# Optimization experiments

Measured on AMD Instinct MI355X. Metric: run time of the kernel, lower is better.

The kernel has to match this reference:

```python
import jax, jax.numpy as jnp
import numpy as np

N = 50000      # nodes
E = 800000     # edges (avg degree 16)
F_IN = 128
HID = 64
NCLS = 40
K = 2          # num_stacks
T = 2          # num_layers (shared weights)


def setup_inputs() -> dict:
    key = jax.random.key(0)
    ks = jax.random.split(key, 10)
    s = 0.05
    return {
        "x": jax.random.normal(ks[0], (N, F_IN), dtype=jnp.float32),
        "edge_index": jax.random.randint(ks[1], (2, E), 0, N),
        "w1_init": jax.random.normal(ks[2], (K, F_IN, HID), dtype=jnp.float32) * s,
        "w1": jax.random.normal(ks[3], (K, HID, HID), dtype=jnp.float32) * s,
        "v1": jax.random.normal(ks[4], (K, F_IN, HID), dtype=jnp.float32) * s,
        "b1": jax.random.normal(ks[5], (K, HID), dtype=jnp.float32) * s,
        "w2_init": jax.random.normal(ks[6], (K, HID, NCLS), dtype=jnp.float32) * s,
        "w2": jax.random.normal(ks[7], (K, NCLS, NCLS), dtype=jnp.float32) * s,
        "v2": jax.random.normal(ks[8], (K, HID, NCLS), dtype=jnp.float32) * s,
        "b2": jax.random.normal(ks[9], (K, NCLS), dtype=jnp.float32) * s,
    }


def _gcn_norm(src, dst, n):
    # PyG gcn_norm with add_self_loops=False: deg over destination, sym norm
    deg = jax.ops.segment_sum(jnp.ones_like(dst, dtype=jnp.float32), dst, num_segments=n)
    dinv = jnp.where(deg > 0, 1.0 / jnp.sqrt(deg), 0.0)
    return dinv[src] * dinv[dst]  # [E]


def _arma_conv(x, src, dst, norm, n, w_init, w, v, b, act):
    # x: [N, Fin]; w_init: [K, Fin, Fout]; w: [K, Fout, Fout]; v: [K, Fin, Fout]; b: [K, Fout]
    root = jnp.einsum('nf,kfg->kng', x, v)  # [K, N, Fout], dropout=0 -> identity
    out = None
    for t in range(T):
        if t == 0:
            h = jnp.einsum('nf,kfg->kng', x, w_init)
        else:
            h = jnp.einsum('knf,kfg->kng', out, w)
        # sparse neighbor aggregation: out[i] = sum_{(j->i)} norm_e * h[j]
        agg = jax.vmap(
            lambda hk: jax.ops.segment_sum(hk[src] * norm[:, None], dst, num_segments=n)
        )(h)  # [K, N, Fout]
        out = act(agg + root + b[:, None, :])
    return out.mean(axis=0)  # mean over stacks -> [N, Fout]


def reference(x, edge_index, w1_init, w1, v1, b1, w2_init, w2, v2, b2):
    src, dst = edge_index[0], edge_index[1]
    norm = _gcn_norm(src, dst, N)
    h = _arma_conv(x, src, dst, norm, N, w1_init, w1, v1, b1, jax.nn.relu)
    h = jax.nn.relu(h)  # wrapper ReLU; dropout is identity in eval
    o = _arma_conv(h, src, dst, norm, N, w2_init, w2, v2, b2, lambda z: z)
    return jax.nn.log_softmax(o, axis=1)
```

## Files before the change

kernel.cpp:

```cpp
#include <hip/hip_runtime.h>
#include <hip/hip_bf16.h>
#include <math.h>

#define N_NODES 50000
#define F_IN 128
#define HID 64
#define NCLS 40
#define K_STACKS 2
#define SCAN_TILE 1024
#define NBLK_CNT 256

typedef __attribute__((ext_vector_type(8))) short short8;
typedef __attribute__((ext_vector_type(4))) float floatx4;
typedef __attribute__((ext_vector_type(2))) float floatx2;

__device__ __forceinline__ unsigned int f32_to_bf16_bits(float f) {
    unsigned int u = __float_as_uint(f);
    return (u + 0x7fffu + ((u >> 16) & 1u)) >> 16;
}
__device__ __forceinline__ unsigned int pack_bf16x2(float a, float b) {
    return f32_to_bf16_bits(a) | (f32_to_bf16_bits(b) << 16);
}
__device__ __forceinline__ unsigned char f32_to_fp8(float v) {
    int pk = __builtin_amdgcn_cvt_pk_fp8_f32(v, v, 0, false);
    return (unsigned char)(pk & 0xff);
}


__global__ __launch_bounds__(256) void count_kernel(const int* __restrict__ dst,
                                                    int* __restrict__ counts,
                                                    int* __restrict__ tileSums, int E) {
    __shared__ int hist[256];
    __shared__ int ts[64];
    int blk = blockIdx.x, t = threadIdx.x;
    hist[t] = 0;
    if (t < 64) ts[t] = 0;
    __syncthreads();
    int chunk = (E + NBLK_CNT - 1) / NBLK_CNT;
    int s = blk * chunk, e = min(E, s + chunk);
    for (int i = s + t; i < e; i += 256) atomicAdd(&hist[dst[i] >> 8], 1);
    __syncthreads();
    counts[t * NBLK_CNT + blk] = hist[t];
    atomicAdd(&ts[t >> 2], hist[t]);
    __syncthreads();
    if (t < 64) atomicAdd(&tileSums[t], ts[t]);
}

__global__ __launch_bounds__(256) void scan_phase3_excl(const int* __restrict__ in,
                                                        const int* __restrict__ tileSums,
                                                        int* __restrict__ out, int n) {
    __shared__ int lds[256];
    __shared__ int tsum[64];
    int b = blockIdx.x, t = threadIdx.x;
    if (t < 64) tsum[t] = tileSums[t];
    int base = b * SCAN_TILE + t * 4;
    int e[4];
    int s = 0;
#pragma unroll
    for (int i = 0; i < 4; ++i) {
        e[i] = (base + i < n) ? in[base + i] : 0;
        s += e[i];
    }
    lds[t] = s;
    __syncthreads();
    int v = s;
    for (int off = 1; off < 256; off <<= 1) {
        int add = (t >= off) ? lds[t - off] : 0;
        __syncthreads();
        v += add;
        lds[t] = v;
        __syncthreads();
    }
    int toff = 0;
    for (int i = 0; i < b; ++i) toff += tsum[i];
    int run = (t == 0 ? 0 : lds[t - 1]) + toff;
#pragma unroll
    for (int i = 0; i < 4; ++i) {
        if (base + i < n) {
            out[base + i] = run;
            run += e[i];
        }
    }
}

__global__ __launch_bounds__(256) void bucket_scatter_kernel(const int* __restrict__ src,
                                                             const int* __restrict__ dst,
                                                             const int* __restrict__ scanned,
                                                             unsigned int* __restrict__ pairs,
                                                             int E) {
    __shared__ int cur[256];
    int blk = blockIdx.x, t = threadIdx.x;
    cur[t] = scanned[t * NBLK_CNT + blk];
    __syncthreads();
    int chunk = (E + NBLK_CNT - 1) / NBLK_CNT;
    int s0 = blk * chunk, e0 = min(E, s0 + chunk);
    for (int i = s0 + t; i < e0; i += 256) {
        int d = dst[i];
        int pos = atomicAdd(&cur[d >> 8], 1);
        pairs[pos] = (unsigned int)src[i] | ((unsigned int)(d & 255) << 16);
    }
}

__global__ __launch_bounds__(256) void csr_build_kernel(const unsigned int* __restrict__ pairs,
                                                        const int* __restrict__ scanned,
                                                        int* __restrict__ row_ptr,
                                                        float* __restrict__ dinv,
                                                        int* __restrict__ col, int N, int E) {
    __shared__ int degl[256], lds[256], curl[256], sb[2];
    int b = blockIdx.x, t = threadIdx.x;
    if (t == 0) {
        sb[0] = scanned[b * NBLK_CNT];
        sb[1] = (b + 1 < 256) ? scanned[(b + 1) * NBLK_CNT] : E;
    }
    degl[t] = 0;
    __syncthreads();
    int bstart = sb[0], bend = sb[1];
    for (int e = bstart + t; e < bend; e += 256) {
        atomicAdd(&degl[(pairs[e] >> 16) & 255], 1);
    }
    __syncthreads();
    int d = degl[t];
    lds[t] = d;
    __syncthreads();
    int v = d;
    for (int off = 1; off < 256; off <<= 1) {
        int add = (t >= off) ? lds[t - off] : 0;
        __syncthreads();
        v += add;
        lds[t] = v;
        __syncthreads();
    }
    int excl = v - d;
    int node = b * 256 + t;
    if (node <= N) row_ptr[node] = bstart + excl;
    if (node < N) dinv[node] = (d > 0) ? (1.0f / sqrtf((float)d)) : 0.0f;
    curl[t] = excl;
    __syncthreads();
    for (int e = bstart + t; e < bend; e += 256) {
        unsigned int p = pairs[e];
        int ln = (p >> 16) & 255;
        int pos = atomicAdd(&curl[ln], 1);
        col[bstart + pos] = (int)(p & 0xffffu);
    }
}

__device__ __forceinline__ void wt_one(const float* __restrict__ in,
                                       unsigned short* __restrict__ out, int li, int C, int F,
                                       int CP) {
    int k = li / (F * CP);
    int r = li - k * F * CP;
    int f = r / CP;
    int c = r - f * CP;
    out[li] = (c < C) ? (unsigned short)f32_to_bf16_bits(in[((size_t)k * C + c) * F + f]) : 0;
}

__global__ void wt_all_kernel(const float* v1, const float* w1i, const float* w1,
                              const float* v2, const float* w2i, const float* w2,
                              unsigned short* v1t, unsigned short* w1it, unsigned short* w1t,
                              unsigned short* v2t, unsigned short* w2it, unsigned short* w2t) {
    int i = blockIdx.x * blockDim.x + threadIdx.x;
    if (i < 16384) wt_one(v1, v1t, i, 128, 64, 128);
    else if (i < 32768) wt_one(w1i, w1it, i - 16384, 128, 64, 128);
    else if (i < 40960) wt_one(w1, w1t, i - 32768, 64, 64, 64);
    else if (i < 46080) wt_one(v2, v2t, i - 40960, 64, 40, 64);
    else if (i < 51200) wt_one(w2i, w2it, i - 46080, 64, 40, 64);
    else if (i < 56320) wt_one(w2, w2t, i - 51200, 40, 40, 64);
}

template <int CINP>
__device__ __forceinline__ void stage_A(const void* A, unsigned short* At, size_t abase,
                                        int n0, int t, int N, int CREAL, int a_bf16) {
    constexpr int CP8 = CINP / 8;
    constexpr int MS = CP8 - 1;
    constexpr int SH = (CP8 == 16) ? 4 : 3;
    for (int i = t; i < 64 * CP8; i += 256) {
        int n = i >> SH;
        int c = i & MS;
        uint4 w = make_uint4(0u, 0u, 0u, 0u);
        int gn = n0 + n;
        if (gn < N && c * 8 < CREAL) {
            if (a_bf16) {
                w = *(const uint4*)((const unsigned short*)A + abase + (size_t)gn * CREAL + c * 8);
            } else {
                const float* srcp = (const float*)A + abase + (size_t)gn * CREAL + c * 8;
                float4 f0 = *(const float4*)(srcp);
                float4 f1 = *(const float4*)(srcp + 4);
                w.x = pack_bf16x2(f0.x, f0.y);
                w.y = pack_bf16x2(f0.z, f0.w);
                w.z = pack_bf16x2(f1.x, f1.y);
                w.w = pack_bf16x2(f1.z, f1.w);
            }
        }
        *(uint4*)(At + n * CINP + ((c ^ (n & MS)) << 3)) = w;
    }
}

template <int CINP>
__device__ __forceinline__ void stage_B(const unsigned short* Bk, unsigned short* Bs, int t,
                                        int COUT) {
    constexpr int CP8 = CINP / 8;
    constexpr int MS = CP8 - 1;
    constexpr int SH = (CP8 == 16) ? 4 : 3;
    for (int i = t; i < COUT * CP8; i += 256) {
        int f = i >> SH;
        int c = i & MS;
        uint4 w = *(const uint4*)(Bk + f * CINP + c * 8);
        *(uint4*)(Bs + f * CINP + ((c ^ (f & MS)) << 3)) = w;
    }
}

template <int CINP>
__global__ __launch_bounds__(256) void gemm_mfma(
    const void* __restrict__ A, const unsigned short* __restrict__ Bt,
    void* __restrict__ out, const float* __restrict__ scale, int N, int COUT, int CREAL,
    int a_per_k, int a_bf16, int out_fp8, int do_scale, int out_inter) {
    constexpr int MS = CINP / 8 - 1;
    __shared__ __align__(16) unsigned short At[64 * CINP];
    __shared__ __align__(16) unsigned short Bs[64 * CINP];

    const int k = blockIdx.y;
    const int n0 = blockIdx.x * 64;
    const int t = threadIdx.x;
    stage_A<CINP>(A, At, a_per_k ? (size_t)k * N * CREAL : (size_t)0, n0, t, N, CREAL, a_bf16);
    stage_B<CINP>(Bt + (size_t)k * COUT * CINP, Bs, t, COUT);
    __syncthreads();

    const int lane = t & 63;
    const int wv = t >> 6;
    const int quad = lane >> 4;
    const int li = lane & 15;
    const int m0 = wv * 16;

    floatx4 acc[4] = {{0.f, 0.f, 0.f, 0.f}, {0.f, 0.f, 0.f, 0.f},
                      {0.f, 0.f, 0.f, 0.f}, {0.f, 0.f, 0.f, 0.f}};
    const int am = (m0 + li) & MS;
#pragma unroll
    for (int kc = 0; kc < CINP / 32; ++kc) {
        int cc = kc * 4 + quad;
        short8 a = *(const short8*)(At + (m0 + li) * CINP + ((cc ^ am) << 3));
#pragma unroll
        for (int nt = 0; nt < 4; ++nt) {
            if (nt * 16 < COUT) {
                int f = nt * 16 + li;
                short8 b = *(const short8*)(Bs + f * CINP + ((cc ^ (f & MS)) << 3));
                acc[nt] = __builtin_amdgcn_mfma_f32_16x16x32_bf16(a, b, acc[nt], 0, 0, 0);
            }
        }
    }

    float sc[4] = {1.f, 1.f, 1.f, 1.f};
    if (do_scale) {
#pragma unroll
        for (int r = 0; r < 4; ++r) {
            int node = n0 + m0 + quad * 4 + r;
            sc[r] = (node < N) ? scale[node] : 1.f;
        }
    }
#pragma unroll
    for (int nt = 0; nt < 4; ++nt) {
        if (nt * 16 >= COUT) continue;
        int f = nt * 16 + li;
        if (f >= COUT) continue;
#pragma unroll
        for (int r = 0; r < 4; ++r) {
            int node = n0 + m0 + quad * 4 + r;
            if (node < N) {
                float val = acc[nt][r] * sc[r];
                if (out_inter) {
                    size_t o = (size_t)node * 2 * COUT + (size_t)k * COUT + f;
                    if (out_fp8)
                        ((unsigned char*)out)[o] = f32_to_fp8(val);
                    else
                        ((unsigned short*)out)[o] = (unsigned short)f32_to_bf16_bits(val);
                } else {
                    size_t o = ((size_t)k * N + node) * COUT + f;
                    ((float*)out)[o] = val;
                }
            }
        }
    }
}

template <int CINP>
__global__ __launch_bounds__(256) void gemm2_mfma(
    const void* __restrict__ A, const unsigned short* __restrict__ Bt1,
    const unsigned short* __restrict__ Bt2, unsigned short* __restrict__ out1,
    unsigned char* __restrict__ out2, const float* __restrict__ scale, int N, int COUT,
    int CREAL, int a_bf16) {
    constexpr int MS = CINP / 8 - 1;
    __shared__ __align__(16) unsigned short At[64 * CINP];
    __shared__ __align__(16) unsigned short Bs1[64 * CINP];
    __shared__ __align__(16) unsigned short Bs2[64 * CINP];

    const int k = blockIdx.y;
    const int n0 = blockIdx.x * 64;
    const int t = threadIdx.x;
    stage_A<CINP>(A, At, (size_t)0, n0, t, N, CREAL, a_bf16);
    stage_B<CINP>(Bt1 + (size_t)k * COUT * CINP, Bs1, t, COUT);
    stage_B<CINP>(Bt2 + (size_t)k * COUT * CINP, Bs2, t, COUT);
    __syncthreads();

    const int lane = t & 63;
    const int wv = t >> 6;
    const int quad = lane >> 4;
    const int li = lane & 15;
    const int m0 = wv * 16;

    floatx4 acc1[4] = {{0.f, 0.f, 0.f, 0.f}, {0.f, 0.f, 0.f, 0.f},
                       {0.f, 0.f, 0.f, 0.f}, {0.f, 0.f, 0.f, 0.f}};
    floatx4 acc2[4] = {{0.f, 0.f, 0.f, 0.f}, {0.f, 0.f, 0.f, 0.f},
                       {0.f, 0.f, 0.f, 0.f}, {0.f, 0.f, 0.f, 0.f}};
    const int am = (m0 + li) & MS;
#pragma unroll
    for (int kc = 0; kc < CINP / 32; ++kc) {
        int cc = kc * 4 + quad;
        short8 a = *(const short8*)(At + (m0 + li) * CINP + ((cc ^ am) << 3));
#pragma unroll
        for (int nt = 0; nt < 4; ++nt) {
            if (nt * 16 < COUT) {
                int f = nt * 16 + li;
                int bo = f * CINP + ((cc ^ (f & MS)) << 3);
                short8 b1 = *(const short8*)(Bs1 + bo);
                short8 b2 = *(const short8*)(Bs2 + bo);
                acc1[nt] = __builtin_amdgcn_mfma_f32_16x16x32_bf16(a, b1, acc1[nt], 0, 0, 0);
                acc2[nt] = __builtin_amdgcn_mfma_f32_16x16x32_bf16(a, b2, acc2[nt], 0, 0, 0);
            }
        }
    }

    float sc[4];
#pragma unroll
    for (int r = 0; r < 4; ++r) {
        int node = n0 + m0 + quad * 4 + r;
        sc[r] = (node < N) ? scale[node] : 1.f;
    }
#pragma unroll
    for (int nt = 0; nt < 4; ++nt) {
        if (nt * 16 >= COUT) continue;
        int f = nt * 16 + li;
        if (f >= COUT) continue;
#pragma unroll
        for (int r = 0; r < 4; ++r) {
            int node = n0 + m0 + quad * 4 + r;
            if (node < N) {
                out1[((size_t)k * N + node) * COUT + f] =
                    (unsigned short)f32_to_bf16_bits(acc1[nt][r]);
                out2[(size_t)node * 2 * COUT + (size_t)k * COUT + f] =
                    f32_to_fp8(acc2[nt][r] * sc[r]);
            }
        }
    }
}

template <int F>
__global__ __launch_bounds__(256) void agg_kernel(
    const unsigned char* __restrict__ h8, const int* __restrict__ row_ptr,
    const int* __restrict__ col, const float* __restrict__ dinv,
    const unsigned short* __restrict__ rootb, const float* __restrict__ bias,
    void* __restrict__ out, int N, int do_relu, int mode) {
    constexpr int FH = F / 8;
    constexpr int ROWB = 2 * F;
    int wid = (blockIdx.x * blockDim.x + threadIdx.x) >> 6;
    int lane = threadIdx.x & 63;
    int half = lane >> 5;
    int l32 = lane & 31;
    int node = wid * 2 + half;
    bool valid = node < N;
    int e0 = 0, deg = 0;
    float dv = 0.f;
    if (valid) {
        e0 = row_ptr[node];
        deg = row_ptr[node + 1] - e0;
        dv = dinv[node];
    }
    const int sub = l32 >> 4;
    const int fq = l32 & 15;
    const int kk = fq >> 3;
    const int fqq = fq & 7;
    const int fqc = (fqq < FH) ? fqq : (FH - 1);
    const int foff = kk * F + fqc * 8;

    float acc[8] = {};
    for (int w0 = 0; w0 < deg; w0 += 32) {
        int mye = w0 + l32;
        int c = (mye < deg) ? col[e0 + mye] : 0;
        int nch = min(deg - w0, 32);
        for (int base = 0; base < nch; base += 16) {
            uint2 v[8];
            float wj[8];
#pragma unroll
            for (int u = 0; u < 8; ++u) {
                int j = base + u * 2 + sub;
                int cj = __shfl(c, (half << 5) | (j & 31));
                bool ok = (j < nch);
                wj[u] = ok ? 1.f : 0.f;
                int cs = ok ? cj : 0;
                v[u] = *(const uint2*)(h8 + (size_t)cs * ROWB + foff);
            }
#pragma unroll
            for (int u = 0; u < 8; ++u) {
                floatx2 f0 = __builtin_amdgcn_cvt_pk_f32_fp8(v[u].x, false);
                floatx2 f1 = __builtin_amdgcn_cvt_pk_f32_fp8(v[u].x, true);
                floatx2 f2 = __builtin_amdgcn_cvt_pk_f32_fp8(v[u].y, false);
                floatx2 f3 = __builtin_amdgcn_cvt_pk_f32_fp8(v[u].y, true);
                acc[0] += wj[u] * f0.x;
                acc[1] += wj[u] * f0.y;
                acc[2] += wj[u] * f1.x;
                acc[3] += wj[u] * f1.y;
                acc[4] += wj[u] * f2.x;
                acc[5] += wj[u] * f2.y;
                acc[6] += wj[u] * f3.x;
                acc[7] += wj[u] * f3.y;
            }
        }
    }
#pragma unroll
    for (int i = 0; i < 8; ++i) acc[i] += __shfl_xor(acc[i], 16);

    size_t oc = ((size_t)kk * N + (valid ? node : 0)) * F + fqc * 8;
    uint4 rv = *(const uint4*)(rootb + oc);
    const float* bp = bias + kk * F + fqc * 8;
    float4 b0 = *(const float4*)(bp);
    float4 b1 = *(const float4*)(bp + 4);
    const unsigned int ru[4] = {rv.x, rv.y, rv.z, rv.w};
    float res[8];
#pragma unroll
    for (int q = 0; q < 4; ++q) {
        float rlo = __uint_as_float(ru[q] << 16);
        float rhi = __uint_as_float(ru[q] & 0xffff0000u);
        float blo = (q < 2) ? ((q == 0) ? b0.x : b0.z) : ((q == 2) ? b1.x : b1.z);
        float bhi = (q < 2) ? ((q == 0) ? b0.y : b0.w) : ((q == 2) ? b1.y : b1.w);
        res[2 * q] = acc[2 * q] * dv + rlo + blo;
        res[2 * q + 1] = acc[2 * q + 1] * dv + rhi + bhi;
    }
    if (do_relu) {
#pragma unroll
        for (int i = 0; i < 8; ++i) res[i] = fmaxf(res[i], 0.f);
    }
    if (mode == 0) {
        if (sub == 0 && fqq < FH && valid) {
            size_t o = ((size_t)kk * N + node) * F + fqq * 8;
            uint4 w;
            w.x = pack_bf16x2(res[0], res[1]);
            w.y = pack_bf16x2(res[2], res[3]);
            w.z = pack_bf16x2(res[4], res[5]);
            w.w = pack_bf16x2(res[6], res[7]);
            *(uint4*)((unsigned short*)out + o) = w;
        }
    } else {
        float mres[8];
#pragma unroll
        for (int i = 0; i < 8; ++i) mres[i] = 0.5f * (res[i] + __shfl_xor(res[i], 8));
        if (mode == 1) {
            if (sub == 0 && kk == 0 && fqq < FH && valid) {
                size_t o = (size_t)node * F + fqq * 8;
                *(float4*)((float*)out + o) = make_float4(mres[0], mres[1], mres[2], mres[3]);
                *(float4*)((float*)out + o + 4) = make_float4(mres[4], mres[5], mres[6], mres[7]);
            }
        } else {
            bool act = (fqq < FH);
            float lm = -INFINITY;
            if (act) {
#pragma unroll
                for (int i = 0; i < 8; ++i) lm = fmaxf(lm, mres[i]);
            }
#pragma unroll
            for (int m = 1; m < 8; m <<= 1) lm = fmaxf(lm, __shfl_xor(lm, m));
            float ls = 0.f;
            if (act) {
#pragma unroll
                for (int i = 0; i < 8; ++i) ls += expf(mres[i] - lm);
            }
#pragma unroll
            for (int m = 1; m < 8; m <<= 1) ls += __shfl_xor(ls, m);
            float lg = lm + logf(ls);
            if (sub == 0 && kk == 0 && act && valid) {
                size_t o = (size_t)node * F + fqq * 8;
                *(float4*)((float*)out + o) =
                    make_float4(mres[0] - lg, mres[1] - lg, mres[2] - lg, mres[3] - lg);
                *(float4*)((float*)out + o + 4) =
                    make_float4(mres[4] - lg, mres[5] - lg, mres[6] - lg, mres[7] - lg);
            }
        }
    }
}


static inline size_t align256(size_t x) { return (x + 255) & ~(size_t)255; }

extern "C" void kernel_launch(void* const* d_in, const int* in_sizes, int n_in,
                              void* d_out, int out_size, void* d_ws, size_t ws_size,
                              hipStream_t stream) {
    const float* x = (const float*)d_in[0];
    const int* ei = (const int*)d_in[1];
    const float* w1_init = (const float*)d_in[2];
    const float* w1 = (const float*)d_in[3];
    const float* v1 = (const float*)d_in[4];
    const float* b1 = (const float*)d_in[5];
    const float* w2_init = (const float*)d_in[6];
    const float* w2 = (const float*)d_in[7];
    const float* v2 = (const float*)d_in[8];
    const float* b2 = (const float*)d_in[9];

    const int N = in_sizes[0] / F_IN;
    const int E = in_sizes[1] / 2;
    const int* src = ei;
    const int* dst = ei + E;

    char* p = (char*)d_ws;
    auto take = [&](size_t bytes) {
        char* r = p;
        p += align256(bytes);
        return r;
    };
    float* dinv = (float*)take((size_t)N * 4);
    int* row_ptr = (int*)take((size_t)(N + 1) * 4);
    int* tileSums = (int*)take(256 * 4);
    int* counts = (int*)take((size_t)256 * NBLK_CNT * 4);
    int* scanned = (int*)take((size_t)256 * NBLK_CNT * 4);
    unsigned int* pairs = (unsigned int*)take((size_t)E * 4);
    int* col = (int*)take((size_t)E * 4);
    unsigned short* v1t = (unsigned short*)take((size_t)2 * 64 * 128 * 2);
    unsigned short* w1it = (unsigned short*)take((size_t)2 * 64 * 128 * 2);
    unsigned short* w1t = (unsigned short*)take((size_t)2 * 64 * 64 * 2);
    unsigned short* v2t = (unsigned short*)take((size_t)2 * 40 * 64 * 2);
    unsigned short* w2it = (unsigned short*)take((size_t)2 * 40 * 64 * 2);
    unsigned short* w2t = (unsigned short*)take((size_t)2 * 40 * 64 * 2);
    unsigned short* rootb = (unsigned short*)take((size_t)K_STACKS * N * HID * 2);
    unsigned char* hb8 = (unsigned char*)take((size_t)K_STACKS * N * HID);
    unsigned short* hc = (unsigned short*)take((size_t)K_STACKS * N * HID * 2);
    float* h1 = (float*)take((size_t)N * HID * 4);

    const int TB = 256;
    const int nCnt = 256 * NBLK_CNT;
    const int nScanBlocks = nCnt / SCAN_TILE;
    const int nBuckets = (N + 255) / 256;
    const int ntiles = (N + 63) / 64;

    hipMemsetAsync(tileSums, 0, 256, stream);
    count_kernel<<<NBLK_CNT, 256, 0, stream>>>(dst, counts, tileSums, E);
    scan_phase3_excl<<<nScanBlocks, 256, 0, stream>>>(counts, tileSums, scanned, nCnt);
    bucket_scatter_kernel<<<NBLK_CNT, 256, 0, stream>>>(src, dst, scanned, pairs, E);
    csr_build_kernel<<<nBuckets, 256, 0, stream>>>(pairs, scanned, row_ptr, dinv, col, N, E);

    wt_all_kernel<<<(56320 + TB - 1) / TB, TB, 0, stream>>>(v1, w1_init, w1, v2, w2_init, w2,
                                                            v1t, w1it, w1t, v2t, w2it, w2t);

    dim3 ggrid(ntiles, K_STACKS);
    const int agg_blocks = ((N + 1) / 2 + 3) / 4;

    gemm2_mfma<128><<<ggrid, 256, 0, stream>>>(x, v1t, w1it, rootb, hb8, dinv, N, HID, 128, 0);
    agg_kernel<HID><<<agg_blocks, 256, 0, stream>>>(hb8, row_ptr, col, dinv, rootb, b1, hc, N, 1, 0);
    gemm_mfma<64><<<ggrid, 256, 0, stream>>>(hc, w1t, hb8, dinv, N, HID, 64, 1, 1, 1, 1, 1);
    agg_kernel<HID><<<agg_blocks, 256, 0, stream>>>(hb8, row_ptr, col, dinv, rootb, b1, h1, N, 1, 1);

    gemm2_mfma<64><<<ggrid, 256, 0, stream>>>(h1, v2t, w2it, rootb, hb8, dinv, N, NCLS, 64, 0);
    agg_kernel<NCLS><<<agg_blocks, 256, 0, stream>>>(hb8, row_ptr, col, dinv, rootb, b2, hc, N, 0, 0);
    gemm_mfma<64><<<ggrid, 256, 0, stream>>>(hc, w2t, hb8, dinv, N, NCLS, 40, 1, 1, 1, 1, 1);
    agg_kernel<NCLS><<<agg_blocks, 256, 0, stream>>>(hb8, row_ptr, col, dinv, rootb, b2,
                                                     (float*)d_out, N, 0, 2);
}
```

Before: 283.3 us.

## Fuse sparse aggregation with following dense GEMMs into per-tile kernels

Replaces separate aggregation and GEMM launches with agg_gemm kernels that gather neighbors for a 64-node tile, apply bias/ReLU (and stack mean), write the result to shared memory as bf16, and then run the next MFMA GEMM in the same block. The first GEMM now loops over both stacks inside a block instead of using a 2D grid, so the A tile is staged once. This removes the intermediate bf16/fp32 round trips through global memory and cuts the launch count from eight to five. In exchange, the aggregation now uses 64-node blocks with more shared memory, which may lower occupancy and load balance for the irregular gather.

```diff
diff --git a/kernel.cpp b/kernel.cpp
--- a/kernel.cpp
+++ b/kernel.cpp
@@ -209,115 +209,39 @@
     }
 }
 
-template <int CINP>
-__global__ __launch_bounds__(256) void gemm_mfma(
-    const void* __restrict__ A, const unsigned short* __restrict__ Bt,
-    void* __restrict__ out, const float* __restrict__ scale, int N, int COUT, int CREAL,
-    int a_per_k, int a_bf16, int out_fp8, int do_scale, int out_inter) {
-    constexpr int MS = CINP / 8 - 1;
+__global__ __launch_bounds__(256) void gemm12_kernel(
+    const float* __restrict__ A, const unsigned short* __restrict__ Bt1,
+    const unsigned short* __restrict__ Bt2, unsigned short* __restrict__ out1,
+    unsigned char* __restrict__ out2, const float* __restrict__ scale, int N) {
+    constexpr int CINP = 128;
+    constexpr int MS = 15;
     __shared__ __align__(16) unsigned short At[64 * CINP];
-    __shared__ __align__(16) unsigned short Bs[64 * CINP];
-
-    const int k = blockIdx.y;
+    __shared__ __align__(16) unsigned short Bs1[64 * CINP];
+    __shared__ __align__(16) unsigned short Bs2[64 * CINP];
     const int n0 = blockIdx.x * 64;
     const int t = threadIdx.x;
-    stage_A<CINP>(A, At, a_per_k ? (size_t)k * N * CREAL : (size_t)0, n0, t, N, CREAL, a_bf16);
-    stage_B<CINP>(Bt + (size_t)k * COUT * CINP, Bs, t, COUT);
-    __syncthreads();
-
+    stage_A<CINP>(A, At, 0, n0, t, N, CINP, 0);
     const int lane = t & 63;
     const int wv = t >> 6;
     const int quad = lane >> 4;
     const int li = lane & 15;
     const int m0 = wv * 16;
-
-    floatx4 acc[4] = {{0.f, 0.f, 0.f, 0.f}, {0.f, 0.f, 0.f, 0.f},
-                      {0.f, 0.f, 0.f, 0.f}, {0.f, 0.f, 0.f, 0.f}};
     const int am = (m0 + li) & MS;
-#pragma unroll
-    for (int kc = 0; kc < CINP / 32; ++kc) {
-        int cc = kc * 4 + quad;
-        short8 a = *(const short8*)(At + (m0 + li) * CINP + ((cc ^ am) << 3));
-#pragma unroll
-        for (int nt = 0; nt < 4; ++nt) {
-            if (nt * 16 < COUT) {
-                int f = nt * 16 + li;
-                short8 b = *(const short8*)(Bs + f * CINP + ((cc ^ (f & MS)) << 3));
-                acc[nt] = __builtin_amdgcn_mfma_f32_16x16x32_bf16(a, b, acc[nt], 0, 0, 0);
-            }
-        }
-    }
-
-    float sc[4] = {1.f, 1.f, 1.f, 1.f};
-    if (do_scale) {
-#pragma unroll
-        for (int r = 0; r < 4; ++r) {
-            int node = n0 + m0 + quad * 4 + r;
-            sc[r] = (node < N) ? scale[node] : 1.f;
-        }
-    }
-#pragma unroll
-    for (int nt = 0; nt < 4; ++nt) {
-        if (nt * 16 >= COUT) continue;
-        int f = nt * 16 + li;
-        if (f >= COUT) continue;
-#pragma unroll
-        for (int r = 0; r < 4; ++r) {
-            int node = n0 + m0 + quad * 4 + r;
-            if (node < N) {
-                float val = acc[nt][r] * sc[r];
-                if (out_inter) {
-                    size_t o = (size_t)node * 2 * COUT + (size_t)k * COUT + f;
-                    if (out_fp8)
-                        ((unsigned char*)out)[o] = f32_to_fp8(val);
-                    else
-                        ((unsigned short*)out)[o] = (unsigned short)f32_to_bf16_bits(val);
-                } else {
-                    size_t o = ((size_t)k * N + node) * COUT + f;
-                    ((float*)out)[o] = val;
-                }
-            }
-        }
-    }
-}
-
-template <int CINP>
-__global__ __launch_bounds__(256) void gemm2_mfma(
-    const void* __restrict__ A, const unsigned short* __restrict__ Bt1,
-    const unsigned short* __restrict__ Bt2, unsigned short* __restrict__ out1,
-    unsigned char* __restrict__ out2, const float* __restrict__ scale, int N, int COUT,
-    int CREAL, int a_bf16) {
-    constexpr int MS = CINP / 8 - 1;
-    __shared__ __align__(16) unsigned short At[64 * CINP];
-    __shared__ __align__(16) unsigned short Bs1[64 * CINP];
-    __shared__ __align__(16) unsigned short Bs2[64 * CINP];
-
-    const int k = blockIdx.y;
-    const int n0 = blockIdx.x * 64;
-    const int t = threadIdx.x;
-    stage_A<CINP>(A, At, (size_t)0, n0, t, N, CREAL, a_bf16);
-    stage_B<CINP>(Bt1 + (size_t)k * COUT * CINP, Bs1, t, COUT);
-    stage_B<CINP>(Bt2 + (size_t)k * COUT * CINP, Bs2, t, COUT);
-    __syncthreads();
-
-    const int lane = t & 63;
-    const int wv = t >> 6;
-    const int quad = lane >> 4;
-    const int li = lane & 15;
-    const int m0 = wv * 16;
-
-    floatx4 acc1[4] = {{0.f, 0.f, 0.f, 0.f}, {0.f, 0.f, 0.f, 0.f},
-                       {0.f, 0.f, 0.f, 0.f}, {0.f, 0.f, 0.f, 0.f}};
-    floatx4 acc2[4] = {{0.f, 0.f, 0.f, 0.f}, {0.f, 0.f, 0.f, 0.f},
-                       {0.f, 0.f, 0.f, 0.f}, {0.f, 0.f, 0.f, 0.f}};
-    const int am = (m0 + li) & MS;
-#pragma unroll
-    for (int kc = 0; kc < CINP / 32; ++kc) {
-        int cc = kc * 4 + quad;
-        short8 a = *(const short8*)(At + (m0 + li) * CINP + ((cc ^ am) << 3));
-#pragma unroll
-        for (int nt = 0; nt < 4; ++nt) {
-            if (nt * 16 < COUT) {
+#pragma unroll 1
+    for (int k = 0; k < 2; ++k) {
+        stage_B<CINP>(Bt1 + (size_t)k * 64 * CINP, Bs1, t, 64);
+        stage_B<CINP>(Bt2 + (size_t)k * 64 * CINP, Bs2, t, 64);
+        __syncthreads();
+        floatx4 acc1[4] = {{0.f, 0.f, 0.f, 0.f}, {0.f, 0.f, 0.f, 0.f},
+                           {0.f, 0.f, 0.f, 0.f}, {0.f, 0.f, 0.f, 0.f}};
+        floatx4 acc2[4] = {{0.f, 0.f, 0.f, 0.f}, {0.f, 0.f, 0.f, 0.f},
+                           {0.f, 0.f, 0.f, 0.f}, {0.f, 0.f, 0.f, 0.f}};
+#pragma unroll
+        for (int kc = 0; kc < 4; ++kc) {
+            int cc = kc * 4 + quad;
+            short8 a = *(const short8*)(At + (m0 + li) * CINP + ((cc ^ am) << 3));
+#pragma unroll
+            for (int nt = 0; nt < 4; ++nt) {
                 int f = nt * 16 + li;
                 int bo = f * CINP + ((cc ^ (f & MS)) << 3);
                 short8 b1 = *(const short8*)(Bs1 + bo);
@@ -326,27 +250,241 @@
                 acc2[nt] = __builtin_amdgcn_mfma_f32_16x16x32_bf16(a, b2, acc2[nt], 0, 0, 0);
             }
         }
-    }
-
-    float sc[4];
-#pragma unroll
-    for (int r = 0; r < 4; ++r) {
-        int node = n0 + m0 + quad * 4 + r;
-        sc[r] = (node < N) ? scale[node] : 1.f;
-    }
-#pragma unroll
-    for (int nt = 0; nt < 4; ++nt) {
-        if (nt * 16 >= COUT) continue;
-        int f = nt * 16 + li;
-        if (f >= COUT) continue;
+        float sc[4];
 #pragma unroll
         for (int r = 0; r < 4; ++r) {
             int node = n0 + m0 + quad * 4 + r;
-            if (node < N) {
-                out1[((size_t)k * N + node) * COUT + f] =
-                    (unsigned short)f32_to_bf16_bits(acc1[nt][r]);
-                out2[(size_t)node * 2 * COUT + (size_t)k * COUT + f] =
-                    f32_to_fp8(acc2[nt][r] * sc[r]);
+            sc[r] = (node < N) ? scale[node] : 1.f;
+        }
+#pragma unroll
+        for (int nt = 0; nt < 4; ++nt) {
+            int f = nt * 16 + li;
+#pragma unroll
+            for (int r = 0; r < 4; ++r) {
+                int node = n0 + m0 + quad * 4 + r;
+                if (node < N) {
+                    out1[((size_t)k * N + node) * 64 + f] =
+                        (unsigned short)f32_to_bf16_bits(acc1[nt][r]);
+                    out2[(size_t)node * 128 + (size_t)k * 64 + f] = f32_to_fp8(acc2[nt][r] * sc[r]);
+                }
+            }
+        }
+        __syncthreads();
+    }
+}
+
+template <int F, int COUT, int FMODE>
+__global__ __launch_bounds__(256) void agg_gemm_kernel(
+    const unsigned char* __restrict__ h8, const int* __restrict__ row_ptr,
+    const int* __restrict__ col, const float* __restrict__ dinv,
+    const unsigned short* __restrict__ rootb, const float* __restrict__ bias,
+    const unsigned short* __restrict__ Bt1, const unsigned short* __restrict__ Bt2,
+    unsigned short* __restrict__ rootOut, unsigned char* __restrict__ tblOut, int N) {
+    constexpr int NA = (FMODE == 1) ? 1 : 2;
+    constexpr int NB = (FMODE == 1) ? 4 : 2;
+    constexpr int BT = COUT * 64;
+    constexpr int NT = (COUT + 15) / 16;
+    constexpr int FH = F / 8;
+    constexpr int ROWB = 2 * F;
+    __shared__ __align__(16) unsigned short At[NA * 64 * 64];
+    __shared__ __align__(16) unsigned short Bs[NB * BT];
+    __shared__ int rp[65];
+    __shared__ float dvl[64];
+
+    const int n0 = blockIdx.x * 64;
+    const int t = threadIdx.x;
+
+    stage_B<64>(Bt1, Bs, t, COUT);
+    stage_B<64>(Bt1 + (size_t)COUT * 64, Bs + BT, t, COUT);
+    if constexpr (FMODE == 1) {
+        stage_B<64>(Bt2, Bs + 2 * BT, t, COUT);
+        stage_B<64>(Bt2 + (size_t)COUT * 64, Bs + 3 * BT, t, COUT);
+    }
+    if (t < 65) rp[t] = row_ptr[min(n0 + t, N)];
+    if (t < 64) dvl[t] = (n0 + t < N) ? dinv[n0 + t] : 0.f;
+    __syncthreads();
+
+    const int lane = t & 63;
+    const int wv = t >> 6;
+    const int half = lane >> 5;
+    const int l32 = lane & 31;
+    const int sub = l32 >> 4;
+    const int fq = l32 & 15;
+    const int kk = fq >> 3;
+    const int fqq = fq & 7;
+    const int fqc = (fqq < FH) ? fqq : (FH - 1);
+    const int foff = kk * F + fqc * 8;
+
+#pragma unroll 1
+    for (int p = 0; p < 8; ++p) {
+        const int nl = wv * 16 + p * 2 + half;
+        const int node = n0 + nl;
+        const bool valid = node < N;
+        const int e0 = rp[nl];
+        const int deg = rp[nl + 1] - e0;
+        const float dv = dvl[nl];
+        float acc[8] = {};
+        for (int w0 = 0; w0 < deg; w0 += 32) {
+            int mye = w0 + l32;
+            int c = (mye < deg) ? col[e0 + mye] : 0;
+            int nch = min(deg - w0, 32);
+            for (int base = 0; base < nch; base += 16) {
+                uint2 v[8];
+                float wj[8];
+#pragma unroll
+                for (int u = 0; u < 8; ++u) {
+                    int j = base + u * 2 + sub;
+                    int cj = __shfl(c, (half << 5) | (j & 31));
+                    bool ok = (j < nch);
+                    wj[u] = ok ? 1.f : 0.f;
+                    int cs = ok ? cj : 0;
+                    v[u] = *(const uint2*)(h8 + (size_t)cs * ROWB + foff);
+                }
+#pragma unroll
+                for (int u = 0; u < 8; ++u) {
+                    floatx2 f0 = __builtin_amdgcn_cvt_pk_f32_fp8(v[u].x, false);
+                    floatx2 f1 = __builtin_amdgcn_cvt_pk_f32_fp8(v[u].x, true);
+                    floatx2 f2 = __builtin_amdgcn_cvt_pk_f32_fp8(v[u].y, false);
+                    floatx2 f3 = __builtin_amdgcn_cvt_pk_f32_fp8(v[u].y, true);
+                    acc[0] += wj[u] * f0.x;
+                    acc[1] += wj[u] * f0.y;
+                    acc[2] += wj[u] * f1.x;
+                    acc[3] += wj[u] * f1.y;
+                    acc[4] += wj[u] * f2.x;
+                    acc[5] += wj[u] * f2.y;
+                    acc[6] += wj[u] * f3.x;
+                    acc[7] += wj[u] * f3.y;
+                }
+            }
+        }
+#pragma unroll
+        for (int i = 0; i < 8; ++i) acc[i] += __shfl_xor(acc[i], 16);
+
+        size_t oc = ((size_t)kk * N + (valid ? node : 0)) * F + fqc * 8;
+        uint4 rv = *(const uint4*)(rootb + oc);
+        const float* bp = bias + kk * F + fqc * 8;
+        float4 b0 = *(const float4*)(bp);
+        float4 b1_ = *(const float4*)(bp + 4);
+        const unsigned int ru[4] = {rv.x, rv.y, rv.z, rv.w};
+        float res[8];
+#pragma unroll
+        for (int q = 0; q < 4; ++q) {
+            float rlo = __uint_as_float(ru[q] << 16);
+            float rhi = __uint_as_float(ru[q] & 0xffff0000u);
+            float blo = (q < 2) ? ((q == 0) ? b0.x : b0.z) : ((q == 2) ? b1_.x : b1_.z);
+            float bhi = (q < 2) ? ((q == 0) ? b0.y : b0.w) : ((q == 2) ? b1_.y : b1_.w);
+            res[2 * q] = acc[2 * q] * dv + rlo + blo;
+            res[2 * q + 1] = acc[2 * q + 1] * dv + rhi + bhi;
+        }
+        if constexpr (FMODE != 2) {
+#pragma unroll
+            for (int i = 0; i < 8; ++i) res[i] = fmaxf(res[i], 0.f);
+        }
+        if constexpr (FMODE == 1) {
+            float mres[8];
+#pragma unroll
+            for (int i = 0; i < 8; ++i) mres[i] = 0.5f * (res[i] + __shfl_xor(res[i], 8));
+            if (sub == 0 && kk == 0) {
+                uint4 w;
+                w.x = pack_bf16x2(mres[0], mres[1]);
+                w.y = pack_bf16x2(mres[2], mres[3]);
+                w.z = pack_bf16x2(mres[4], mres[5]);
+                w.w = pack_bf16x2(mres[6], mres[7]);
+                *(uint4*)(At + nl * 64 + ((fqq ^ (nl & 7)) << 3)) = w;
+            }
+        } else {
+            if (sub == 0) {
+                uint4 w = make_uint4(0u, 0u, 0u, 0u);
+                if (fqq < FH) {
+                    w.x = pack_bf16x2(res[0], res[1]);
+                    w.y = pack_bf16x2(res[2], res[3]);
+                    w.z = pack_bf16x2(res[4], res[5]);
+                    w.w = pack_bf16x2(res[6], res[7]);
+                }
+                *(uint4*)(At + kk * 4096 + nl * 64 + ((fqq ^ (nl & 7)) << 3)) = w;
+            }
+        }
+    }
+    __syncthreads();
+
+    const int quad = lane >> 4;
+    const int li = lane & 15;
+    const int m0 = wv * 16;
+    const int am = (m0 + li) & 7;
+
+    if constexpr (FMODE == 1) {
+        floatx4 aR[2][NT] = {};
+        floatx4 aT[2][NT] = {};
+#pragma unroll
+        for (int kc = 0; kc < 2; ++kc) {
+            int cc = kc * 4 + quad;
+            short8 a = *(const short8*)(At + (m0 + li) * 64 + ((cc ^ am) << 3));
+#pragma unroll
+            for (int nt = 0; nt < NT; ++nt) {
+                int f = nt * 16 + li;
+                int fc = (COUT & 15) ? ((f < COUT) ? f : (COUT - 1)) : f;
+                int bo = fc * 64 + ((cc ^ (fc & 7)) << 3);
+#pragma unroll
+                for (int k = 0; k < 2; ++k) {
+                    short8 bR = *(const short8*)(Bs + k * BT + bo);
+                    short8 bT = *(const short8*)(Bs + (2 + k) * BT + bo);
+                    aR[k][nt] = __builtin_amdgcn_mfma_f32_16x16x32_bf16(a, bR, aR[k][nt], 0, 0, 0);
+                    aT[k][nt] = __builtin_amdgcn_mfma_f32_16x16x32_bf16(a, bT, aT[k][nt], 0, 0, 0);
+                }
+            }
+        }
+#pragma unroll
+        for (int k = 0; k < 2; ++k) {
+#pragma unroll
+            for (int nt = 0; nt < NT; ++nt) {
+                int f = nt * 16 + li;
+                if (f >= COUT) continue;
+#pragma unroll
+                for (int r = 0; r < 4; ++r) {
+                    int nl2 = m0 + quad * 4 + r;
+                    int node = n0 + nl2;
+                    if (node < N) {
+                        rootOut[((size_t)k * N + node) * COUT + f] =
+                            (unsigned short)f32_to_bf16_bits(aR[k][nt][r]);
+                        tblOut[(size_t)node * 2 * COUT + (size_t)k * COUT + f] =
+                            f32_to_fp8(aT[k][nt][r] * dvl[nl2]);
+                    }
+                }
+            }
+        }
+    } else {
+        floatx4 ac[2][NT] = {};
+#pragma unroll
+        for (int kc = 0; kc < 2; ++kc) {
+            int cc = kc * 4 + quad;
+            int ao = (m0 + li) * 64 + ((cc ^ am) << 3);
+            short8 a0 = *(const short8*)(At + ao);
+            short8 a1 = *(const short8*)(At + 4096 + ao);
+#pragma unroll
+            for (int nt = 0; nt < NT; ++nt) {
+                int f = nt * 16 + li;
+                int fc = (COUT & 15) ? ((f < COUT) ? f : (COUT - 1)) : f;
+                int bo = fc * 64 + ((cc ^ (fc & 7)) << 3);
+                short8 b0 = *(const short8*)(Bs + bo);
+                short8 b1v = *(const short8*)(Bs + BT + bo);
+                ac[0][nt] = __builtin_amdgcn_mfma_f32_16x16x32_bf16(a0, b0, ac[0][nt], 0, 0, 0);
+                ac[1][nt] = __builtin_amdgcn_mfma_f32_16x16x32_bf16(a1, b1v, ac[1][nt], 0, 0, 0);
+            }
+        }
+#pragma unroll
+        for (int k = 0; k < 2; ++k) {
+#pragma unroll
+            for (int nt = 0; nt < NT; ++nt) {
+                int f = nt * 16 + li;
+                if (f >= COUT) continue;
+#pragma unroll
+                for (int r = 0; r < 4; ++r) {
+                    int nl2 = m0 + quad * 4 + r;
+                    int node = n0 + nl2;
+                    if (node < N)
+                        tblOut[(size_t)node * 2 * COUT + (size_t)k * COUT + f] =
+                            f32_to_fp8(ac[k][nt][r] * dvl[nl2]);
+                }
             }
         }
     }
@@ -527,9 +665,9 @@
     unsigned short* w2it = (unsigned short*)take((size_t)2 * 40 * 64 * 2);
     unsigned short* w2t = (unsigned short*)take((size_t)2 * 40 * 64 * 2);
     unsigned short* rootb = (unsigned short*)take((size_t)K_STACKS * N * HID * 2);
-    unsigned char* hb8 = (unsigned char*)take((size_t)K_STACKS * N * HID);
-    unsigned short* hc = (unsigned short*)take((size_t)K_STACKS * N * HID * 2);
-    float* h1 = (float*)take((size_t)N * HID * 4);
+    unsigned short* root2 = (unsigned short*)take((size_t)K_STACKS * N * NCLS * 2);
+    unsigned char* tblA = (unsigned char*)take((size_t)K_STACKS * N * HID);
+    unsigned char* tblB = (unsigned char*)take((size_t)K_STACKS * N * HID);
 
     const int TB = 256;
     const int nCnt = 256 * NBLK_CNT;
@@ -546,17 +684,18 @@
     wt_all_kernel<<<(56320 + TB - 1) / TB, TB, 0, stream>>>(v1, w1_init, w1, v2, w2_init, w2,
                                                             v1t, w1it, w1t, v2t, w2it, w2t);
 
-    dim3 ggrid(ntiles, K_STACKS);
     const int agg_blocks = ((N + 1) / 2 + 3) / 4;
 
-    gemm2_mfma<128><<<ggrid, 256, 0, stream>>>(x, v1t, w1it, rootb, hb8, dinv, N, HID, 128, 0);
-    agg_kernel<HID><<<agg_blocks, 256, 0, stream>>>(hb8, row_ptr, col, dinv, rootb, b1, hc, N, 1, 0);
-    gemm_mfma<64><<<ggrid, 256, 0, stream>>>(hc, w1t, hb8, dinv, N, HID, 64, 1, 1, 1, 1, 1);
-    agg_kernel<HID><<<agg_blocks, 256, 0, stream>>>(hb8, row_ptr, col, dinv, rootb, b1, h1, N, 1, 1);
-
-    gemm2_mfma<64><<<ggrid, 256, 0, stream>>>(h1, v2t, w2it, rootb, hb8, dinv, N, NCLS, 64, 0);
-    agg_kernel<NCLS><<<agg_blocks, 256, 0, stream>>>(hb8, row_ptr, col, dinv, rootb, b2, hc, N, 0, 0);
-    gemm_mfma<64><<<ggrid, 256, 0, stream>>>(hc, w2t, hb8, dinv, N, NCLS, 40, 1, 1, 1, 1, 1);
-    agg_kernel<NCLS><<<agg_blocks, 256, 0, stream>>>(hb8, row_ptr, col, dinv, rootb, b2,
+    gemm12_kernel<<<ntiles, 256, 0, stream>>>(x, v1t, w1it, rootb, tblA, dinv, N);
+    agg_gemm_kernel<HID, HID, 0><<<ntiles, 256, 0, stream>>>(
+        tblA, row_ptr, col, dinv, rootb, b1, w1t, nullptr, nullptr, tblB, N);
+
+    agg_gemm_kernel<HID, NCLS, 1><<<ntiles, 256, 0, stream>>>(
+        tblB, row_ptr, col, dinv, rootb, b1, v2t, w2it, root2, tblA, N);
+
+    agg_gemm_kernel<NCLS, NCLS, 2><<<ntiles, 256, 0, stream>>>(
+        tblA, row_ptr, col, dinv, root2, b2, w2t, nullptr, nullptr, tblB, N);
+
+    agg_kernel<NCLS><<<agg_blocks, 256, 0, stream>>>(tblB, row_ptr, col, dinv, root2, b2,
                                                      (float*)d_out, N, 0, 2);
 }
```

Result: slower. 302.3 us (+6.7%).
